# Performance work log

Hardware: AMD Instinct MI355X
Metric: run time of the kernel (lower is better)

## Reference

```python
import jax, jax.numpy as jnp
from jax import lax
import numpy as np

N_CLUSTERS = 8
G_CLUSTERS = 2
D_DIM = 512
DN = ('NCHW', 'OIHW', 'NCHW')


def _conv(x, w, b):
    y = lax.conv_general_dilated(x, w, window_strides=(1, 1), padding='VALID',
                                 dimension_numbers=DN)
    return y + b[None, :, None, None]


def setup_inputs() -> dict:
    key = jax.random.key(0)
    ks = jax.random.split(key, 6)
    B, D, H, W = 32, D_DIM, 7, 250
    KG = N_CLUSTERS + G_CLUSTERS
    scale = 1.0 / np.sqrt(D * 7)
    return {
        'x': jax.random.normal(ks[0], (B, D, H, W), dtype=jnp.float32),
        'feat_w': jax.random.normal(ks[1], (D, D, 7, 1), dtype=jnp.float32) * scale,
        'feat_b': jax.random.normal(ks[2], (D,), dtype=jnp.float32) * 0.01,
        'assign_w': jax.random.normal(ks[3], (KG, D, 7, 1), dtype=jnp.float32) * scale,
        'assign_b': jax.random.normal(ks[4], (KG,), dtype=jnp.float32) * 0.01,
        'centroids': jax.random.uniform(ks[5], (D, KG), dtype=jnp.float32),
    }


def reference(x, feat_w, feat_b, assign_w, assign_b, centroids):
    # features branch: conv(7,1) + ReLU -> (B, D, H', W)
    feat = jnp.maximum(_conv(x, feat_w, feat_b), 0.0)
    # assignment branch: conv(7,1) -> softmax over clusters -> (B, K+G, H', W)
    soft = jax.nn.softmax(_conv(x, assign_w, assign_b), axis=1)
    # Fused VLAD aggregation (mathematically identical to
    # sum_hw soft[b,k,hw] * (feat[b,d,hw] - centroids[d,k]) without
    # materializing the (B,D,K+G,H',W) residual tensor):
    s_sum = soft.sum(axis=(-2, -1))                                # (B, K+G)
    agg = jnp.einsum('bkhw,bdhw->bdk', soft, feat)                 # (B, D, K+G)
    cluster_res = agg - centroids[None, :, :] * s_sum[:, None, :]  # (B, D, K+G)
    cluster_res = cluster_res[..., :N_CLUSTERS]                    # drop ghost clusters
    # L2 normalize over feature dim (torch F.normalize, eps=1e-12)
    norm = jnp.sqrt(jnp.sum(cluster_res * cluster_res, axis=1, keepdims=True))
    cluster_l2 = cluster_res / jnp.maximum(norm, 1e-12)
    # (B, D, K) -> (B, K, D) -> (B, K*D)
    out = jnp.swapaxes(cluster_l2, 1, 2).reshape(x.shape[0], N_CLUSTERS * D_DIM)
    return out
```

## Files before the change

### kernel.cpp

```cpp
#include <hip/hip_runtime.h>
#include <stdint.h>

typedef float f32x4 __attribute__((ext_vector_type(4)));
typedef __bf16 bf16x8 __attribute__((ext_vector_type(8)));
typedef unsigned short ushortx8 __attribute__((ext_vector_type(8)));

#define D_DIM 512
#define KGC 10
#define NCLU 8
#define BATCH 32
#define WPOS 250
#define WPAD 256
#define KDIM 3584
#define MROWS 522
#define MPAD 528
#define MBIG 544
#define MH 272
#define BN 128
#define KSPLIT 4
#define KCHUNK 896
#define NS 14
#define NT 64

__device__ __forceinline__ float bf2f(unsigned short u) {
  union { unsigned int i; float f; } v; v.i = ((unsigned int)u) << 16; return v.f;
}
__device__ __forceinline__ unsigned short f2bf(float f) {
  union { float f; unsigned int i; } v; v.f = f;
  unsigned int r = v.i + 0x7FFFu + ((v.i >> 16) & 1u);
  return (unsigned short)(r >> 16);
}

__device__ __forceinline__ void load_lds16(const void* g, void* l) {
  __builtin_amdgcn_global_load_lds(
      (const __attribute__((address_space(1))) void*)g,
      (__attribute__((address_space(3))) void*)l, 16, 0, 0);
}

__global__ void prep_kernel(const float* __restrict__ fw,
                            const float* __restrict__ fb,
                            const float* __restrict__ aw,
                            const float* __restrict__ ab,
                            unsigned short* __restrict__ Wcat,
                            float* __restrict__ bcat) {
  int r = blockIdx.x;
  unsigned short* dst = Wcat + (size_t)r * KDIM;
  const float* src = (r < D_DIM) ? (fw + (size_t)r * KDIM)
                   : (r < MROWS) ? (aw + (size_t)(r - D_DIM) * KDIM)
                                 : nullptr;
  for (int i = threadIdx.x; i < KDIM / 4; i += 256) {
    unsigned short o0 = 0, o1 = 0, o2 = 0, o3 = 0;
    if (src) {
      float4 v = ((const float4*)src)[i];
      o0 = f2bf(v.x); o1 = f2bf(v.y); o2 = f2bf(v.z); o3 = f2bf(v.w);
    }
    ushort4 o; o.x = o0; o.y = o1; o.z = o2; o.w = o3;
    ((ushort4*)dst)[i] = o;
  }
  if (threadIdx.x == 0)
    bcat[r] = r < D_DIM ? fb[r] : (r < MROWS ? ab[r - D_DIM] : 0.f);
}

__global__ __launch_bounds__(512, 4) void gemm_fused(
    const float* __restrict__ x, const unsigned short* __restrict__ Wcat,
    float* __restrict__ P) {
  __shared__ __align__(16) unsigned short Wl[MH * 64];
  __shared__ __align__(16) unsigned short Xl[BN * 64];
  const int tid = threadIdx.x;
  const int nt = blockIdx.x, mh = blockIdx.y, sp = blockIdx.z;
  const int lane = tid & 63, wv = tid >> 6;
  const int fr = lane & 15, kg = lane >> 4;
  const int sx = fr & 7;
  const int nloc = tid & 127, oc = tid >> 7;
  const int nglob = nt * BN + nloc;
  const int b = nglob >> 8, ncol = nglob & 255;
  const bool okn = ncol < WPOS;
  const float* xb = x + (size_t)b * KDIM * WPOS + ncol;
  const int kbase = sp * KCHUNK;
  const unsigned short* Wg = Wcat + (size_t)mh * MH * KDIM + kbase;

  float xr[16];
  auto loadx = [&](int st) {
#pragma unroll
    for (int pass = 0; pass < 2; pass++) {
      int k0 = kbase + st * 64 + (oc + 4 * pass) * 8;
#pragma unroll
      for (int e = 0; e < 8; e++)
        xr[pass * 8 + e] = okn ? xb[(size_t)(k0 + e) * WPOS] : 0.f;
    }
  };

  f32x4 acc[17];
  const f32x4 zero = {0.f, 0.f, 0.f, 0.f};
#pragma unroll
  for (int f = 0; f < 17; f++) acc[f] = zero;

  loadx(0);

  for (int st = 0; st < NS; st++) {
    __syncthreads();
#pragma unroll
    for (int it = 0; it < 5; it++) {
      int s = it * 512 + tid;
      if (s < MH * 8) {
        int row = s >> 3, p = s & 7;
        int blk = p ^ (row & 7);
        load_lds16(Wg + (size_t)row * KDIM + st * 64 + blk * 8, &Wl[s * 8]);
      }
    }
#pragma unroll
    for (int pass = 0; pass < 2; pass++) {
      int oct = oc + 4 * pass;
      ushortx8 pk;
#pragma unroll
      for (int e = 0; e < 8; e++) pk[e] = f2bf(xr[pass * 8 + e]);
      *(ushortx8*)&Xl[nloc * 64 + (oct ^ (nloc & 7)) * 8] = pk;
    }
    __syncthreads();
    if (st + 1 < NS) loadx(st + 1);
#pragma unroll
    for (int ks = 0; ks < 2; ks++) {
      const int off = ((ks * 4 + kg) ^ sx) * 8;
      bf16x8 bfr = *(const bf16x8*)&Xl[(wv * 16 + fr) * 64 + off];
#pragma unroll
      for (int f = 0; f < 17; f++) {
        bf16x8 af = *(const bf16x8*)&Wl[(f * 16 + fr) * 64 + off];
        acc[f] = __builtin_amdgcn_mfma_f32_16x16x32_bf16(af, bfr, acc[f], 0, 0, 0);
      }
    }
  }

  float* Pb = P + (size_t)(((sp * 2 + mh) * NT) + nt) * (MH * BN);
  const int n = wv * 16 + fr;
#pragma unroll
  for (int f = 0; f < 17; f++) {
    const int m = f * 16 + kg * 4;
#pragma unroll
    for (int r = 0; r < 4; r++)
      Pb[(size_t)(m + r) * BN + n] = acc[f][r];
  }
}

__global__ __launch_bounds__(256) void reduce_kernel(
    const float* __restrict__ P, const float* __restrict__ bcat,
    unsigned short* __restrict__ Y) {
  const int nt = blockIdx.x, mg = blockIdx.y;
  const int t = threadIdx.x;
  const int m = mg * 16 + (t >> 4);
  const int nl = (t & 15) * 8;
  if (m >= MPAD) return;
  const int mh = m >= MH, ml = m - mh * MH;
  const size_t slice = (size_t)MH * BN;
  const size_t base = (size_t)ml * BN + nl;
  float s[8];
#pragma unroll
  for (int e = 0; e < 8; e++) s[e] = 0.f;
#pragma unroll
  for (int sp = 0; sp < KSPLIT; sp++) {
    const float* p = P + ((size_t)((sp * 2 + mh) * NT) + nt) * slice + base;
    float4 a = *(const float4*)p;
    float4 c = *(const float4*)(p + 4);
    s[0] += a.x; s[1] += a.y; s[2] += a.z; s[3] += a.w;
    s[4] += c.x; s[5] += c.y; s[6] += c.z; s[7] += c.w;
  }
  float bias = bcat[m];
  ushortx8 o;
#pragma unroll
  for (int e = 0; e < 8; e++) {
    float v = s[e] + bias;
    if (m < D_DIM) v = fmaxf(v, 0.f);
    o[e] = f2bf(v);
  }
  const int nglob = nt * BN + nl;
  const int bb = nglob >> 8, col = nglob & 255;
  *(ushortx8*)&Y[(size_t)bb * MPAD * WPAD + (size_t)m * WPAD + col] = o;
}

__global__ __launch_bounds__(256) void epi_kernel(
    const unsigned short* __restrict__ Y, const float* __restrict__ cent,
    float* __restrict__ out) {
  __shared__ float soft[WPAD];
  __shared__ float red[4];
  const int b = blockIdx.x >> 3, k = blockIdx.x & 7;
  const int tid = threadIdx.x;
  const unsigned short* Yb = Y + (size_t)b * MPAD * WPAD;

  float sv = 0.f;
  if (tid < WPOS) {
    float lg[KGC];
    float mx = -1e30f;
#pragma unroll
    for (int j = 0; j < KGC; j++) {
      lg[j] = bf2f(Yb[(size_t)(D_DIM + j) * WPAD + tid]);
      mx = fmaxf(mx, lg[j]);
    }
    float s = 0.f, ek = 0.f;
#pragma unroll
    for (int j = 0; j < KGC; j++) {
      float e = __expf(lg[j] - mx);
      s += e;
      if (j == k) ek = e;
    }
    sv = ek / s;
  }
  soft[tid] = sv;
  __syncthreads();

  float v = sv;
#pragma unroll
  for (int o = 32; o > 0; o >>= 1) v += __shfl_down(v, o, 64);
  if ((tid & 63) == 0) red[tid >> 6] = v;
  __syncthreads();
  float ssum = red[0] + red[1] + red[2] + red[3];

  float a0 = 0.f, a1 = 0.f;
  const unsigned short* row0 = Yb + (size_t)tid * WPAD;
  const unsigned short* row1 = Yb + (size_t)(tid + 256) * WPAD;
  for (int w = 0; w < WPAD; w += 8) {
    ushortx8 f0 = *(const ushortx8*)(row0 + w);
    ushortx8 f1 = *(const ushortx8*)(row1 + w);
#pragma unroll
    for (int u = 0; u < 8; u++) {
      float s = soft[w + u];
      a0 += bf2f(f0[u]) * s;
      a1 += bf2f(f1[u]) * s;
    }
  }
  float c0 = a0 - cent[(size_t)tid * KGC + k] * ssum;
  float c1 = a1 - cent[(size_t)(tid + 256) * KGC + k] * ssum;

  __syncthreads();
  float q = c0 * c0 + c1 * c1;
#pragma unroll
  for (int o = 32; o > 0; o >>= 1) q += __shfl_down(q, o, 64);
  if ((tid & 63) == 0) red[tid >> 6] = q;
  __syncthreads();
  float norm = sqrtf(red[0] + red[1] + red[2] + red[3]);
  float inv = 1.f / fmaxf(norm, 1e-12f);

  float* ob = out + (size_t)b * (NCLU * D_DIM) + (size_t)k * D_DIM;
  ob[tid] = c0 * inv;
  ob[tid + 256] = c1 * inv;
}

extern "C" void kernel_launch(void* const* d_in, const int* in_sizes, int n_in,
                              void* d_out, int out_size, void* d_ws, size_t ws_size,
                              hipStream_t stream) {
  const float* x  = (const float*)d_in[0];
  const float* fw = (const float*)d_in[1];
  const float* fb = (const float*)d_in[2];
  const float* aw = (const float*)d_in[3];
  const float* ab = (const float*)d_in[4];
  const float* ce = (const float*)d_in[5];
  float* out = (float*)d_out;
  char* ws = (char*)d_ws;

  const size_t WC_BYTES = (size_t)MBIG * KDIM * 2;
  const size_t BC_BYTES = 4096;
  const size_t P_BYTES  = (size_t)KSPLIT * 2 * NT * MH * BN * 4;
  unsigned short* Wc = (unsigned short*)(ws);
  float*          bc = (float*)(ws + WC_BYTES);
  float*          P  = (float*)(ws + WC_BYTES + BC_BYTES);
  unsigned short* Yv = (unsigned short*)(ws + WC_BYTES + BC_BYTES + P_BYTES);

  prep_kernel<<<MBIG, 256, 0, stream>>>(fw, fb, aw, ab, Wc, bc);
  gemm_fused<<<dim3(NT, 2, KSPLIT), 512, 0, stream>>>(x, Wc, P);
  reduce_kernel<<<dim3(NT, 34), 256, 0, stream>>>(P, bc, Yv);
  epi_kernel<<<BATCH * NCLU, 256, 0, stream>>>(Yv, ce, out);
}
```

Baseline: 235.0 us.

## Drop split-K partials and fuse bias/ReLU epilogue into retiled GEMM

The GEMM is retiled from a 272x128 tile with 4-way split-K into a full-K 160x64 tile with a 2x2 wave layout, using 512 blocks ordered with an XCD-aware swizzle. Bias, ReLU and the bf16 store are now done directly in the GEMM epilogue, so the fp32 partial-sum buffer and the separate reduce kernel are gone. This removes a large round trip of partials through global memory and one launch. In exchange each block runs a much longer K loop with less parallelism per output, and the weight padding grows to 640 rows, which costs extra wasted MFMA work.

```diff
diff --git a/kernel.cpp b/kernel.cpp
--- a/kernel.cpp
+++ b/kernel.cpp
@@ -14,13 +14,12 @@
 #define KDIM 3584
 #define MROWS 522
 #define MPAD 528
-#define MBIG 544
-#define MH 272
-#define BN 128
-#define KSPLIT 4
-#define KCHUNK 896
-#define NS 14
-#define NT 64
+#define MBIG 640
+#define BM 160
+#define BN 64
+#define NS 56
+#define NTB 128
+#define MSB 4
 
 __device__ __forceinline__ float bf2f(unsigned short u) {
   union { unsigned int i; float f; } v; v.i = ((unsigned int)u) << 16; return v.f;
@@ -61,39 +60,41 @@
     bcat[r] = r < D_DIM ? fb[r] : (r < MROWS ? ab[r - D_DIM] : 0.f);
 }
 
-__global__ __launch_bounds__(512, 4) void gemm_fused(
+__global__ __launch_bounds__(256, 2) void gemm_fused(
     const float* __restrict__ x, const unsigned short* __restrict__ Wcat,
-    float* __restrict__ P) {
-  __shared__ __align__(16) unsigned short Wl[MH * 64];
+    const float* __restrict__ bcat, unsigned short* __restrict__ Y) {
+  __shared__ __align__(16) unsigned short Wl[BM * 64];
   __shared__ __align__(16) unsigned short Xl[BN * 64];
   const int tid = threadIdx.x;
-  const int nt = blockIdx.x, mh = blockIdx.y, sp = blockIdx.z;
+  const int hw = blockIdx.x;
+  const int work = (hw & 7) * 64 + (hw >> 3);
+  const int nt = work >> 2, ms = work & 3;
   const int lane = tid & 63, wv = tid >> 6;
+  const int wm = wv >> 1, wn = wv & 1;
   const int fr = lane & 15, kg = lane >> 4;
   const int sx = fr & 7;
-  const int nloc = tid & 127, oc = tid >> 7;
+  const int nloc = tid & 63, oc = tid >> 6;
   const int nglob = nt * BN + nloc;
   const int b = nglob >> 8, ncol = nglob & 255;
   const bool okn = ncol < WPOS;
   const float* xb = x + (size_t)b * KDIM * WPOS + ncol;
-  const int kbase = sp * KCHUNK;
-  const unsigned short* Wg = Wcat + (size_t)mh * MH * KDIM + kbase;
+  const unsigned short* Wg = Wcat + (size_t)ms * BM * KDIM;
 
   float xr[16];
   auto loadx = [&](int st) {
 #pragma unroll
     for (int pass = 0; pass < 2; pass++) {
-      int k0 = kbase + st * 64 + (oc + 4 * pass) * 8;
+      int k0 = st * 64 + (oc + 4 * pass) * 8;
 #pragma unroll
       for (int e = 0; e < 8; e++)
         xr[pass * 8 + e] = okn ? xb[(size_t)(k0 + e) * WPOS] : 0.f;
     }
   };
 
-  f32x4 acc[17];
+  f32x4 acc[5][2];
   const f32x4 zero = {0.f, 0.f, 0.f, 0.f};
 #pragma unroll
-  for (int f = 0; f < 17; f++) acc[f] = zero;
+  for (int f = 0; f < 5; f++) { acc[f][0] = zero; acc[f][1] = zero; }
 
   loadx(0);
 
@@ -101,12 +102,10 @@
     __syncthreads();
 #pragma unroll
     for (int it = 0; it < 5; it++) {
-      int s = it * 512 + tid;
-      if (s < MH * 8) {
-        int row = s >> 3, p = s & 7;
-        int blk = p ^ (row & 7);
-        load_lds16(Wg + (size_t)row * KDIM + st * 64 + blk * 8, &Wl[s * 8]);
-      }
+      int s = it * 256 + tid;
+      int row = s >> 3, p = s & 7;
+      int blk = p ^ (row & 7);
+      load_lds16(Wg + (size_t)row * KDIM + st * 64 + blk * 8, &Wl[s * 8]);
     }
 #pragma unroll
     for (int pass = 0; pass < 2; pass++) {
@@ -121,59 +120,37 @@
 #pragma unroll
     for (int ks = 0; ks < 2; ks++) {
       const int off = ((ks * 4 + kg) ^ sx) * 8;
-      bf16x8 bfr = *(const bf16x8*)&Xl[(wv * 16 + fr) * 64 + off];
-#pragma unroll
-      for (int f = 0; f < 17; f++) {
-        bf16x8 af = *(const bf16x8*)&Wl[(f * 16 + fr) * 64 + off];
-        acc[f] = __builtin_amdgcn_mfma_f32_16x16x32_bf16(af, bfr, acc[f], 0, 0, 0);
+      bf16x8 b0 = *(const bf16x8*)&Xl[(wn * 32 + fr) * 64 + off];
+      bf16x8 b1 = *(const bf16x8*)&Xl[(wn * 32 + 16 + fr) * 64 + off];
+#pragma unroll
+      for (int f = 0; f < 5; f++) {
+        bf16x8 af = *(const bf16x8*)&Wl[(wm * 80 + f * 16 + fr) * 64 + off];
+        acc[f][0] = __builtin_amdgcn_mfma_f32_16x16x32_bf16(af, b0, acc[f][0], 0, 0, 0);
+        acc[f][1] = __builtin_amdgcn_mfma_f32_16x16x32_bf16(af, b1, acc[f][1], 0, 0, 0);
       }
     }
   }
 
-  float* Pb = P + (size_t)(((sp * 2 + mh) * NT) + nt) * (MH * BN);
-  const int n = wv * 16 + fr;
-#pragma unroll
-  for (int f = 0; f < 17; f++) {
-    const int m = f * 16 + kg * 4;
-#pragma unroll
-    for (int r = 0; r < 4; r++)
-      Pb[(size_t)(m + r) * BN + n] = acc[f][r];
-  }
-}
-
-__global__ __launch_bounds__(256) void reduce_kernel(
-    const float* __restrict__ P, const float* __restrict__ bcat,
-    unsigned short* __restrict__ Y) {
-  const int nt = blockIdx.x, mg = blockIdx.y;
-  const int t = threadIdx.x;
-  const int m = mg * 16 + (t >> 4);
-  const int nl = (t & 15) * 8;
-  if (m >= MPAD) return;
-  const int mh = m >= MH, ml = m - mh * MH;
-  const size_t slice = (size_t)MH * BN;
-  const size_t base = (size_t)ml * BN + nl;
-  float s[8];
-#pragma unroll
-  for (int e = 0; e < 8; e++) s[e] = 0.f;
-#pragma unroll
-  for (int sp = 0; sp < KSPLIT; sp++) {
-    const float* p = P + ((size_t)((sp * 2 + mh) * NT) + nt) * slice + base;
-    float4 a = *(const float4*)p;
-    float4 c = *(const float4*)(p + 4);
-    s[0] += a.x; s[1] += a.y; s[2] += a.z; s[3] += a.w;
-    s[4] += c.x; s[5] += c.y; s[6] += c.z; s[7] += c.w;
-  }
-  float bias = bcat[m];
-  ushortx8 o;
-#pragma unroll
-  for (int e = 0; e < 8; e++) {
-    float v = s[e] + bias;
-    if (m < D_DIM) v = fmaxf(v, 0.f);
-    o[e] = f2bf(v);
-  }
-  const int nglob = nt * BN + nl;
-  const int bb = nglob >> 8, col = nglob & 255;
-  *(ushortx8*)&Y[(size_t)bb * MPAD * WPAD + (size_t)m * WPAD + col] = o;
+  const int bb = (nt * BN) >> 8;
+  const int cbase = (nt * BN) & 255;
+  unsigned short* Yb = Y + (size_t)bb * MPAD * WPAD;
+#pragma unroll
+  for (int f = 0; f < 5; f++) {
+    const int m0 = ms * BM + wm * 80 + f * 16 + kg * 4;
+#pragma unroll
+    for (int nf = 0; nf < 2; nf++) {
+      const int c = cbase + wn * 32 + nf * 16 + fr;
+#pragma unroll
+      for (int r = 0; r < 4; r++) {
+        const int m = m0 + r;
+        if (m < MPAD) {
+          float v = acc[f][nf][r] + bcat[m];
+          if (m < D_DIM) v = fmaxf(v, 0.f);
+          Yb[(size_t)m * WPAD + c] = f2bf(v);
+        }
+      }
+    }
+  }
 }
 
 __global__ __launch_bounds__(256) void epi_kernel(
@@ -257,14 +234,11 @@
 
   const size_t WC_BYTES = (size_t)MBIG * KDIM * 2;
   const size_t BC_BYTES = 4096;
-  const size_t P_BYTES  = (size_t)KSPLIT * 2 * NT * MH * BN * 4;
   unsigned short* Wc = (unsigned short*)(ws);
   float*          bc = (float*)(ws + WC_BYTES);
-  float*          P  = (float*)(ws + WC_BYTES + BC_BYTES);
-  unsigned short* Yv = (unsigned short*)(ws + WC_BYTES + BC_BYTES + P_BYTES);
+  unsigned short* Yv = (unsigned short*)(ws + WC_BYTES + BC_BYTES);
 
   prep_kernel<<<MBIG, 256, 0, stream>>>(fw, fb, aw, ab, Wc, bc);
-  gemm_fused<<<dim3(NT, 2, KSPLIT), 512, 0, stream>>>(x, Wc, P);
-  reduce_kernel<<<dim3(NT, 34), 256, 0, stream>>>(P, bc, Yv);
+  gemm_fused<<<NTB * MSB, 256, 0, stream>>>(x, Wc, bc, Yv);
   epi_kernel<<<BATCH * NCLU, 256, 0, stream>>>(Yv, ce, out);
 }
```

New measurement: 268.2 us. 14.1% more time.

## Retile GEMM waves to 2x4 grid and widen epilogue to 512 threads

Applied to the files above, without the earlier changes.

The GEMM wave layout changes from 8 waves each covering all 17 M-fragments for one 16-column N slice to a 2x4 grid. Each wave now covers 9 M-fragments by two N fragments, so each A fragment read from LDS feeds two MFMAs. This halves LDS A reads per MFMA but pads M from 544 to 576 rows, adding wasted compute and a larger partial buffer. The epilogue uses 512 threads with one feature row each and vectorized soft reads, and the reduce grid grows to cover the new padding.

```diff
diff --git a/kernel.cpp b/kernel.cpp
--- a/kernel.cpp
+++ b/kernel.cpp
@@ -14,8 +14,8 @@
 #define KDIM 3584
 #define MROWS 522
 #define MPAD 528
-#define MBIG 544
-#define MH 272
+#define MBIG 576
+#define MHB 288
 #define BN 128
 #define KSPLIT 4
 #define KCHUNK 896
@@ -64,11 +64,12 @@
 __global__ __launch_bounds__(512, 4) void gemm_fused(
     const float* __restrict__ x, const unsigned short* __restrict__ Wcat,
     float* __restrict__ P) {
-  __shared__ __align__(16) unsigned short Wl[MH * 64];
+  __shared__ __align__(16) unsigned short Wl[MHB * 64];
   __shared__ __align__(16) unsigned short Xl[BN * 64];
   const int tid = threadIdx.x;
   const int nt = blockIdx.x, mh = blockIdx.y, sp = blockIdx.z;
   const int lane = tid & 63, wv = tid >> 6;
+  const int wm = wv >> 2, wn = wv & 3;
   const int fr = lane & 15, kg = lane >> 4;
   const int sx = fr & 7;
   const int nloc = tid & 127, oc = tid >> 7;
@@ -77,7 +78,7 @@
   const bool okn = ncol < WPOS;
   const float* xb = x + (size_t)b * KDIM * WPOS + ncol;
   const int kbase = sp * KCHUNK;
-  const unsigned short* Wg = Wcat + (size_t)mh * MH * KDIM + kbase;
+  const unsigned short* Wg = Wcat + (size_t)mh * MHB * KDIM + kbase;
 
   float xr[16];
   auto loadx = [&](int st) {
@@ -90,10 +91,10 @@
     }
   };
 
-  f32x4 acc[17];
+  f32x4 acc[9][2];
   const f32x4 zero = {0.f, 0.f, 0.f, 0.f};
 #pragma unroll
-  for (int f = 0; f < 17; f++) acc[f] = zero;
+  for (int f = 0; f < 9; f++) { acc[f][0] = zero; acc[f][1] = zero; }
 
   loadx(0);
 
@@ -102,7 +103,7 @@
 #pragma unroll
     for (int it = 0; it < 5; it++) {
       int s = it * 512 + tid;
-      if (s < MH * 8) {
+      if (s < MHB * 8) {
         int row = s >> 3, p = s & 7;
         int blk = p ^ (row & 7);
         load_lds16(Wg + (size_t)row * KDIM + st * 64 + blk * 8, &Wl[s * 8]);
@@ -121,23 +122,28 @@
 #pragma unroll
     for (int ks = 0; ks < 2; ks++) {
       const int off = ((ks * 4 + kg) ^ sx) * 8;
-      bf16x8 bfr = *(const bf16x8*)&Xl[(wv * 16 + fr) * 64 + off];
-#pragma unroll
-      for (int f = 0; f < 17; f++) {
-        bf16x8 af = *(const bf16x8*)&Wl[(f * 16 + fr) * 64 + off];
-        acc[f] = __builtin_amdgcn_mfma_f32_16x16x32_bf16(af, bfr, acc[f], 0, 0, 0);
+      bf16x8 b0 = *(const bf16x8*)&Xl[(wn * 32 + fr) * 64 + off];
+      bf16x8 b1 = *(const bf16x8*)&Xl[(wn * 32 + 16 + fr) * 64 + off];
+#pragma unroll
+      for (int f = 0; f < 9; f++) {
+        bf16x8 af = *(const bf16x8*)&Wl[(wm * 144 + f * 16 + fr) * 64 + off];
+        acc[f][0] = __builtin_amdgcn_mfma_f32_16x16x32_bf16(af, b0, acc[f][0], 0, 0, 0);
+        acc[f][1] = __builtin_amdgcn_mfma_f32_16x16x32_bf16(af, b1, acc[f][1], 0, 0, 0);
       }
     }
   }
 
-  float* Pb = P + (size_t)(((sp * 2 + mh) * NT) + nt) * (MH * BN);
-  const int n = wv * 16 + fr;
-#pragma unroll
-  for (int f = 0; f < 17; f++) {
-    const int m = f * 16 + kg * 4;
-#pragma unroll
-    for (int r = 0; r < 4; r++)
-      Pb[(size_t)(m + r) * BN + n] = acc[f][r];
+  float* Pb = P + (size_t)(((sp * 2 + mh) * NT) + nt) * (MHB * BN);
+#pragma unroll
+  for (int f = 0; f < 9; f++) {
+    const int m = wm * 144 + f * 16 + kg * 4;
+#pragma unroll
+    for (int nf = 0; nf < 2; nf++) {
+      const int n = wn * 32 + nf * 16 + fr;
+#pragma unroll
+      for (int r = 0; r < 4; r++)
+        Pb[(size_t)(m + r) * BN + n] = acc[f][nf][r];
+    }
   }
 }
 
@@ -149,8 +155,8 @@
   const int m = mg * 16 + (t >> 4);
   const int nl = (t & 15) * 8;
   if (m >= MPAD) return;
-  const int mh = m >= MH, ml = m - mh * MH;
-  const size_t slice = (size_t)MH * BN;
+  const int mh = m >= MHB, ml = m - mh * MHB;
+  const size_t slice = (size_t)MHB * BN;
   const size_t base = (size_t)ml * BN + nl;
   float s[8];
 #pragma unroll
@@ -176,11 +182,11 @@
   *(ushortx8*)&Y[(size_t)bb * MPAD * WPAD + (size_t)m * WPAD + col] = o;
 }
 
-__global__ __launch_bounds__(256) void epi_kernel(
+__global__ __launch_bounds__(512) void epi_kernel(
     const unsigned short* __restrict__ Y, const float* __restrict__ cent,
     float* __restrict__ out) {
   __shared__ float soft[WPAD];
-  __shared__ float red[4];
+  __shared__ float red[8];
   const int b = blockIdx.x >> 3, k = blockIdx.x & 7;
   const int tid = threadIdx.x;
   const unsigned short* Yb = Y + (size_t)b * MPAD * WPAD;
@@ -203,7 +209,7 @@
     }
     sv = ek / s;
   }
-  soft[tid] = sv;
+  if (tid < WPAD) soft[tid] = sv;
   __syncthreads();
 
   float v = sv;
@@ -211,36 +217,44 @@
   for (int o = 32; o > 0; o >>= 1) v += __shfl_down(v, o, 64);
   if ((tid & 63) == 0) red[tid >> 6] = v;
   __syncthreads();
-  float ssum = red[0] + red[1] + red[2] + red[3];
-
-  float a0 = 0.f, a1 = 0.f;
-  const unsigned short* row0 = Yb + (size_t)tid * WPAD;
-  const unsigned short* row1 = Yb + (size_t)(tid + 256) * WPAD;
+  float ssum = 0.f;
+#pragma unroll
+  for (int i = 0; i < 8; i++) ssum += red[i];
+
+  float a[8];
+#pragma unroll
+  for (int u = 0; u < 8; u++) a[u] = 0.f;
+  const unsigned short* row = Yb + (size_t)tid * WPAD;
   for (int w = 0; w < WPAD; w += 8) {
-    ushortx8 f0 = *(const ushortx8*)(row0 + w);
-    ushortx8 f1 = *(const ushortx8*)(row1 + w);
-#pragma unroll
-    for (int u = 0; u < 8; u++) {
-      float s = soft[w + u];
-      a0 += bf2f(f0[u]) * s;
-      a1 += bf2f(f1[u]) * s;
-    }
-  }
-  float c0 = a0 - cent[(size_t)tid * KGC + k] * ssum;
-  float c1 = a1 - cent[(size_t)(tid + 256) * KGC + k] * ssum;
-
-  __syncthreads();
-  float q = c0 * c0 + c1 * c1;
+    ushortx8 f0 = *(const ushortx8*)(row + w);
+    float4 s0 = *(const float4*)&soft[w];
+    float4 s1 = *(const float4*)&soft[w + 4];
+    a[0] += bf2f(f0[0]) * s0.x;
+    a[1] += bf2f(f0[1]) * s0.y;
+    a[2] += bf2f(f0[2]) * s0.z;
+    a[3] += bf2f(f0[3]) * s0.w;
+    a[4] += bf2f(f0[4]) * s1.x;
+    a[5] += bf2f(f0[5]) * s1.y;
+    a[6] += bf2f(f0[6]) * s1.z;
+    a[7] += bf2f(f0[7]) * s1.w;
+  }
+  float asum = ((a[0] + a[1]) + (a[2] + a[3])) + ((a[4] + a[5]) + (a[6] + a[7]));
+  float c = asum - cent[(size_t)tid * KGC + k] * ssum;
+
+  __syncthreads();
+  float q = c * c;
 #pragma unroll
   for (int o = 32; o > 0; o >>= 1) q += __shfl_down(q, o, 64);
   if ((tid & 63) == 0) red[tid >> 6] = q;
   __syncthreads();
-  float norm = sqrtf(red[0] + red[1] + red[2] + red[3]);
+  float nsum = 0.f;
+#pragma unroll
+  for (int i = 0; i < 8; i++) nsum += red[i];
+  float norm = sqrtf(nsum);
   float inv = 1.f / fmaxf(norm, 1e-12f);
 
   float* ob = out + (size_t)b * (NCLU * D_DIM) + (size_t)k * D_DIM;
-  ob[tid] = c0 * inv;
-  ob[tid + 256] = c1 * inv;
+  ob[tid] = c * inv;
 }
 
 extern "C" void kernel_launch(void* const* d_in, const int* in_sizes, int n_in,
@@ -257,7 +271,7 @@
 
   const size_t WC_BYTES = (size_t)MBIG * KDIM * 2;
   const size_t BC_BYTES = 4096;
-  const size_t P_BYTES  = (size_t)KSPLIT * 2 * NT * MH * BN * 4;
+  const size_t P_BYTES  = (size_t)KSPLIT * 2 * NT * MHB * BN * 4;
   unsigned short* Wc = (unsigned short*)(ws);
   float*          bc = (float*)(ws + WC_BYTES);
   float*          P  = (float*)(ws + WC_BYTES + BC_BYTES);
@@ -265,6 +279,6 @@
 
   prep_kernel<<<MBIG, 256, 0, stream>>>(fw, fb, aw, ab, Wc, bc);
   gemm_fused<<<dim3(NT, 2, KSPLIT), 512, 0, stream>>>(x, Wc, P);
-  reduce_kernel<<<dim3(NT, 34), 256, 0, stream>>>(P, bc, Yv);
-  epi_kernel<<<BATCH * NCLU, 256, 0, stream>>>(Yv, ce, out);
-}
+  reduce_kernel<<<dim3(NT, 36), 256, 0, stream>>>(P, bc, Yv);
+  epi_kernel<<<BATCH * NCLU, 512, 0, stream>>>(Yv, ce, out);
+}
```

After: 245.8 us. +4.6%, slower.
